# Performance work log

Hardware: AMD Instinct MI355X
Metric: run time of the kernel (lower is better)

Reference implementation:

```python
import jax, jax.numpy as jnp
import numpy as np

NUM_HEADS = 12


def setup_inputs() -> dict:
    key = jax.random.key(0)
    k0, k1, k2 = jax.random.split(key, 3)
    B, S, D = 2, 2048, 1536
    scale = 1.0 / np.sqrt(D)
    return {
        "hidden_states": jax.random.normal(k0, (B, S, D), dtype=jnp.float32),
        "W_fc": jax.random.normal(k1, (D, D), dtype=jnp.float32) * scale,
        "b_fc": jnp.zeros((D,), dtype=jnp.float32),
        "W_proj": jax.random.normal(k2, (D, D), dtype=jnp.float32) * scale,
        "b_proj": jnp.zeros((D,), dtype=jnp.float32),
    }


def reference(hidden_states, W_fc, b_fc, W_proj, b_proj):
    B, S, D = hidden_states.shape
    H = NUM_HEADS
    hd = D // H
    # value_states: [B, H, S, hd] (key_states == value_states in the original)
    v = (hidden_states @ W_fc.T + b_fc).reshape(B, S, H, hd).transpose(0, 2, 1, 3)
    # Uniform-weight causal sliding-window attention, window_h = 2^(h+1)-1.
    i = jnp.arange(S)[:, None]          # query pos
    j = jnp.arange(S)[None, :]          # key pos
    w = (2 ** jnp.arange(1, H + 1, dtype=jnp.int32) - 1)[:, None, None]  # [H,1,1]
    mask = (j <= i) & (j >= i - w + 1)                                    # [H,S,S]
    valid_len = jnp.minimum(i + 1, w).astype(v.dtype)                     # [H,S,1]
    attn = jnp.where(mask, 1.0 / valid_len, 0.0)                          # [H,S,S]
    # [H,S,S] x [B,H,S,hd] -> [B,S,H,hd] -> [B,S,D]
    out = jnp.einsum("hqk,bhkd->bqhd", attn, v).reshape(B, S, D)
    attn_weights = jnp.broadcast_to(attn[None], (B, H, S, S))
    return out @ W_proj.T + b_proj, attn_weights
```

## Files before the change

### kernel.cpp

```cpp
#include <hip/hip_runtime.h>
#include <hip/hip_bf16.h>

#define S_LEN   2048
#define DMODEL  1536
#define NBATCH  2
#define NHEADS  12
#define MROWS   (NBATCH * S_LEN)
#define NCHUNK  64
#define CHUNK   32

typedef unsigned short u16;
typedef __attribute__((ext_vector_type(8))) short bf16x8;
typedef __attribute__((ext_vector_type(4))) float f32x4;

__device__ __forceinline__ u16 f2bf(float x) {
  unsigned u = __float_as_uint(x);
  u += 0x7fffu + ((u >> 16) & 1u);
  return (u16)(u >> 16);
}
__device__ __forceinline__ float bf2f(u16 x) {
  return __uint_as_float(((unsigned)x) << 16);
}

#define N4_HID  1572864
#define N4_W    589824
__global__ void cvt_all(const float4* __restrict__ h, const float4* __restrict__ wf,
                        const float4* __restrict__ wp, ushort4* __restrict__ ho,
                        ushort4* __restrict__ wfo, ushort4* __restrict__ wpo) {
  int t = blockIdx.x * blockDim.x + threadIdx.x;
  const float4* src;
  ushort4* dst;
  int idx;
  if (t < N4_HID)            { src = h;  dst = ho;  idx = t; }
  else if (t < N4_HID + N4_W){ src = wf; dst = wfo; idx = t - N4_HID; }
  else                       { src = wp; dst = wpo; idx = t - N4_HID - N4_W; }
  float4 f = src[idx];
  ushort4 o;
  o.x = f2bf(f.x); o.y = f2bf(f.y); o.z = f2bf(f.z); o.w = f2bf(f.w);
  dst[idx] = o;
}

__device__ __forceinline__ void gld_lds16(u16* lds, const u16* g) {
  __builtin_amdgcn_global_load_lds(
      (const __attribute__((address_space(1))) unsigned int*)g,
      (__attribute__((address_space(3))) unsigned int*)lds, 16, 0, 0);
}

template <bool WITH_CSUM, typename CT>
__global__ __launch_bounds__(256)
void gemm_bt_bias(const u16* __restrict__ A, const u16* __restrict__ B,
                  const float* __restrict__ bias, CT* __restrict__ C,
                  float* __restrict__ cs, int Ndim, int Kdim) {
  __shared__ __align__(16) u16 As[128 * 32];
  __shared__ __align__(16) u16 Bs[128 * 32];
  __shared__ float colpart[4][128];

  const int tid  = threadIdx.x;
  const int wave = tid >> 6;
  const int lane = tid & 63;
  const int l15  = lane & 15;
  const int quad = lane >> 4;
  const int bm = blockIdx.y * 128;
  const int bn = blockIdx.x * 128;
  const int wm = (wave >> 1) * 64;
  const int wn = (wave & 1) * 64;

  f32x4 acc[4][4] = {};

  const int srow = wave * 32 + (lane >> 2);
  const int skk  = (lane & 3) * 8;
  const u16* gA = A + (size_t)(bm + srow) * Kdim + skk;
  const u16* gB = B + (size_t)(bn + srow) * Kdim + skk;
  u16* lA = &As[(wave * 32) * 32];
  u16* lB = &Bs[(wave * 32) * 32];
  const size_t rstep16 = (size_t)16 * Kdim;

  for (int k0 = 0; k0 < Kdim; k0 += 32) {
    gld_lds16(lA,           gA + k0);
    gld_lds16(lA + 16 * 32, gA + k0 + rstep16);
    gld_lds16(lB,           gB + k0);
    gld_lds16(lB + 16 * 32, gB + k0 + rstep16);
    __syncthreads();

    bf16x8 af[4], bfr[4];
#pragma unroll
    for (int i = 0; i < 4; ++i)
      af[i] = *(const bf16x8*)&As[(wm + i * 16 + l15) * 32 + quad * 8];
#pragma unroll
    for (int j = 0; j < 4; ++j)
      bfr[j] = *(const bf16x8*)&Bs[(wn + j * 16 + l15) * 32 + quad * 8];
#pragma unroll
    for (int i = 0; i < 4; ++i)
#pragma unroll
      for (int j = 0; j < 4; ++j)
        acc[i][j] = __builtin_amdgcn_mfma_f32_16x16x32_bf16(af[i], bfr[j], acc[i][j], 0, 0, 0);
    __syncthreads();
  }

  const int r0 = quad * 4;
#pragma unroll
  for (int j = 0; j < 4; ++j) {
    const int col = bn + wn + j * 16 + l15;
    const float bj = bias[col];
    float sA = 0.f, sB = 0.f;
#pragma unroll
    for (int i = 0; i < 4; ++i) {
      const int row = bm + wm + i * 16 + r0;
#pragma unroll
      for (int r = 0; r < 4; ++r) {
        float cv = acc[i][j][r] + bj;
        if constexpr (sizeof(CT) == 2)
          C[(size_t)(row + r) * Ndim + col] = (CT)f2bf(cv);
        else
          C[(size_t)(row + r) * Ndim + col] = (CT)cv;
        if (WITH_CSUM) { if (i < 2) sA += cv; else sB += cv; }
      }
    }
    if (WITH_CSUM) {
      sA += __shfl_xor(sA, 16); sA += __shfl_xor(sA, 32);
      sB += __shfl_xor(sB, 16); sB += __shfl_xor(sB, 32);
      if (quad == 0) {
        colpart[(wm >> 5) | 0][wn + j * 16 + l15] = sA;
        colpart[(wm >> 5) | 1][wn + j * 16 + l15] = sB;
      }
    }
  }
  if (WITH_CSUM) {
    __syncthreads();
    if (tid < 128) {
      const int b  = bm >> 11;
      const int c0 = (bm & 2047) >> 5;
#pragma unroll
      for (int g = 0; g < 4; ++g)
        cs[((size_t)b * NCHUNK + c0 + g) * DMODEL + bn + tid] = colpart[g][tid];
    }
  }
}

__global__ void chunk_prefix(const float* __restrict__ cs, float* __restrict__ E) {
  int t = blockIdx.x * blockDim.x + threadIdx.x;
  int d = t % DMODEL;
  int c = (t / DMODEL) % NCHUNK;
  int b = t / (DMODEL * NCHUNK);
  const float* p = cs + (size_t)b * NCHUNK * DMODEL + d;
  float s = 0.f;
  for (int cc = 0; cc < c; ++cc) s += p[(size_t)cc * DMODEL];
  E[t] = s;
}

__global__ void winavg_strip(const u16* __restrict__ v, const float* __restrict__ E,
                             u16* __restrict__ A2) {
  int t = blockIdx.x * blockDim.x + threadIdx.x;
  int d = t % DMODEL;
  int s = (t / DMODEL) & 255;
  int b = t / (DMODEL * 256);
  const int h = d >> 7;
  const int w = (2 << h) - 1;
  const u16* vb  = v + (size_t)b * S_LEN * DMODEL + d;
  const float* Eb = E + (size_t)b * NCHUNK * DMODEL + d;

  const int i0 = s * 8;
  float lead = Eb[(size_t)(i0 >> 5) * DMODEL];
  for (int r = i0 & ~31; r < i0; ++r)
    lead += bf2f(vb[(size_t)r * DMODEL]);

  float trail = 0.f;
  if (i0 + 7 >= w) {
    const int jf = max(i0, w) - w;
    if (jf > 0) {
      const int ct = (jf - 1) >> 5;
      trail = Eb[(size_t)ct * DMODEL];
      for (int r = ct * 32; r < jf; ++r)
        trail += bf2f(vb[(size_t)r * DMODEL]);
    }
  }

  u16* out = A2 + ((size_t)(b * S_LEN + i0)) * DMODEL + d;
#pragma unroll
  for (int rr = 0; rr < 8; ++rr) {
    const int i = i0 + rr;
    lead += bf2f(vb[(size_t)i * DMODEL]);
    float o;
    if (i < w) {
      o = lead / (float)(i + 1);
    } else {
      trail += bf2f(vb[(size_t)(i - w) * DMODEL]);
      o = (lead - trail) / (float)w;
    }
    out[(size_t)rr * DMODEL] = f2bf(o);
  }
}

__global__ void attn_weights_kernel(f32x4* __restrict__ out4) {
  int t = blockIdx.x * blockDim.x + threadIdx.x;
  int j0 = (t & 511) << 2;
  int i  = (t >> 9) & (S_LEN - 1);
  int bh = t >> 20;
  int h  = bh >= NHEADS ? bh - NHEADS : bh;
  int w  = (2 << h) - 1;
  int len = min(i + 1, w);
  float inv = 1.0f / (float)len;
  int lo = i - w + 1;
  f32x4 r;
  r.x = (j0     <= i && j0     >= lo) ? inv : 0.f;
  r.y = (j0 + 1 <= i && j0 + 1 >= lo) ? inv : 0.f;
  r.z = (j0 + 2 <= i && j0 + 2 >= lo) ? inv : 0.f;
  r.w = (j0 + 3 <= i && j0 + 3 >= lo) ? inv : 0.f;
  __builtin_nontemporal_store(r, &out4[t]);
}

extern "C" void kernel_launch(void* const* d_in, const int* in_sizes, int n_in,
                              void* d_out, int out_size, void* d_ws, size_t ws_size,
                              hipStream_t stream) {
  const float* hidden = (const float*)d_in[0];
  const float* W_fc   = (const float*)d_in[1];
  const float* b_fc   = (const float*)d_in[2];
  const float* W_proj = (const float*)d_in[3];
  const float* b_proj = (const float*)d_in[4];
  float* outp = (float*)d_out;

  char* ws = (char*)d_ws;
  u16*   A16   = (u16*)(ws);
  u16*   Wfc16 = (u16*)(ws + 12582912);
  u16*   Wpj16 = (u16*)(ws + 17301504);
  u16*   v16   = (u16*)(ws + 22020096);
  float* csums = (float*)(ws + 34603008);
  float* Epre  = (float*)(ws + 35389440);

  cvt_all<<<10752, 256, 0, stream>>>((const float4*)hidden, (const float4*)W_fc,
                                     (const float4*)W_proj, (ushort4*)A16,
                                     (ushort4*)Wfc16, (ushort4*)Wpj16);

  gemm_bt_bias<true, u16><<<dim3(DMODEL / 128, MROWS / 128), 256, 0, stream>>>(
      A16, Wfc16, b_fc, v16, csums, DMODEL, DMODEL);

  chunk_prefix<<<(NBATCH * NCHUNK * DMODEL) / 256, 256, 0, stream>>>(csums, Epre);

  winavg_strip<<<(NBATCH * (S_LEN / 8) * DMODEL) / 256, 256, 0, stream>>>(v16, Epre, A16);

  gemm_bt_bias<false, float><<<dim3(DMODEL / 128, MROWS / 128), 256, 0, stream>>>(
      A16, Wpj16, b_proj, outp, nullptr, DMODEL, DMODEL);

  attn_weights_kernel<<<(NBATCH * NHEADS * S_LEN * S_LEN / 4) / 256, 256, 0, stream>>>(
      (f32x4*)(outp + (size_t)MROWS * DMODEL));
}
```

Measured before the change: 574.6 us.

## Fuse attention-weights fill into both GEMM launches as extra blocks

Drops the standalone attention-weights kernel and appends 3072 extra blocks to each GEMM launch; these extra blocks run a grid-stride loop that writes half of the 400MB attention-weight tensor each. The goal is to overlap the bandwidth-bound weight writes with the compute-bound GEMMs and save one launch. GEMM tile indices move to a 1D grid. The risk is that store traffic competes with the GEMM loads, and scheduling may place the weight blocks after the GEMM blocks instead of alongside them.

New measurement: 541.1 us. 5.8% less time.

```diff
diff --git a/kernel.cpp b/kernel.cpp
--- a/kernel.cpp
+++ b/kernel.cpp
@@ -8,6 +8,11 @@
 #define MROWS   (NBATCH * S_LEN)
 #define NCHUNK  64
 #define CHUNK   32
+
+#define NGEMM_BLK  384
+#define AW_BLK     3072
+#define AW_TOTAL4  25165824u
+#define AW_HALF4   12582912u
 
 typedef unsigned short u16;
 typedef __attribute__((ext_vector_type(8))) short bf16x8;
@@ -48,9 +53,33 @@
 
 template <bool WITH_CSUM, typename CT>
 __global__ __launch_bounds__(256)
-void gemm_bt_bias(const u16* __restrict__ A, const u16* __restrict__ B,
-                  const float* __restrict__ bias, CT* __restrict__ C,
-                  float* __restrict__ cs, int Ndim, int Kdim) {
+void gemm_aw(const u16* __restrict__ A, const u16* __restrict__ B,
+             const float* __restrict__ bias, CT* __restrict__ C,
+             float* __restrict__ cs, f32x4* __restrict__ aw,
+             unsigned aw0, unsigned awcnt, int Ndim, int Kdim) {
+  if ((int)blockIdx.x >= NGEMM_BLK) {
+    const unsigned stride = (gridDim.x - NGEMM_BLK) * 256u;
+    const unsigned end = aw0 + awcnt;
+    unsigned t = aw0 + (blockIdx.x - NGEMM_BLK) * 256u + threadIdx.x;
+    for (; t < end; t += stride) {
+      int j0 = (int)(t & 511u) << 2;
+      int i  = (int)(t >> 9) & (S_LEN - 1);
+      int bh = (int)(t >> 20);
+      int h  = bh >= NHEADS ? bh - NHEADS : bh;
+      int w  = (2 << h) - 1;
+      int len = min(i + 1, w);
+      float inv = 1.0f / (float)len;
+      int lo = i - w + 1;
+      f32x4 r;
+      r.x = (j0     <= i && j0     >= lo) ? inv : 0.f;
+      r.y = (j0 + 1 <= i && j0 + 1 >= lo) ? inv : 0.f;
+      r.z = (j0 + 2 <= i && j0 + 2 >= lo) ? inv : 0.f;
+      r.w = (j0 + 3 <= i && j0 + 3 >= lo) ? inv : 0.f;
+      __builtin_nontemporal_store(r, &aw[t]);
+    }
+    return;
+  }
+
   __shared__ __align__(16) u16 As[128 * 32];
   __shared__ __align__(16) u16 Bs[128 * 32];
   __shared__ float colpart[4][128];
@@ -60,8 +89,8 @@
   const int lane = tid & 63;
   const int l15  = lane & 15;
   const int quad = lane >> 4;
-  const int bm = blockIdx.y * 128;
-  const int bn = blockIdx.x * 128;
+  const int bm = (blockIdx.x / (DMODEL / 128)) * 128;
+  const int bn = (blockIdx.x % (DMODEL / 128)) * 128;
   const int wm = (wave >> 1) * 64;
   const int wn = (wave & 1) * 64;
 
@@ -191,24 +220,6 @@
   }
 }
 
-__global__ void attn_weights_kernel(f32x4* __restrict__ out4) {
-  int t = blockIdx.x * blockDim.x + threadIdx.x;
-  int j0 = (t & 511) << 2;
-  int i  = (t >> 9) & (S_LEN - 1);
-  int bh = t >> 20;
-  int h  = bh >= NHEADS ? bh - NHEADS : bh;
-  int w  = (2 << h) - 1;
-  int len = min(i + 1, w);
-  float inv = 1.0f / (float)len;
-  int lo = i - w + 1;
-  f32x4 r;
-  r.x = (j0     <= i && j0     >= lo) ? inv : 0.f;
-  r.y = (j0 + 1 <= i && j0 + 1 >= lo) ? inv : 0.f;
-  r.z = (j0 + 2 <= i && j0 + 2 >= lo) ? inv : 0.f;
-  r.w = (j0 + 3 <= i && j0 + 3 >= lo) ? inv : 0.f;
-  __builtin_nontemporal_store(r, &out4[t]);
-}
-
 extern "C" void kernel_launch(void* const* d_in, const int* in_sizes, int n_in,
                               void* d_out, int out_size, void* d_ws, size_t ws_size,
                               hipStream_t stream) {
@@ -218,6 +229,7 @@
   const float* W_proj = (const float*)d_in[3];
   const float* b_proj = (const float*)d_in[4];
   float* outp = (float*)d_out;
+  f32x4* aw = (f32x4*)(outp + (size_t)MROWS * DMODEL);
 
   char* ws = (char*)d_ws;
   u16*   A16   = (u16*)(ws);
@@ -231,16 +243,13 @@
                                      (const float4*)W_proj, (ushort4*)A16,
                                      (ushort4*)Wfc16, (ushort4*)Wpj16);
 
-  gemm_bt_bias<true, u16><<<dim3(DMODEL / 128, MROWS / 128), 256, 0, stream>>>(
-      A16, Wfc16, b_fc, v16, csums, DMODEL, DMODEL);
+  gemm_aw<true, u16><<<NGEMM_BLK + AW_BLK, 256, 0, stream>>>(
+      A16, Wfc16, b_fc, v16, csums, aw, 0u, AW_HALF4, DMODEL, DMODEL);
 
   chunk_prefix<<<(NBATCH * NCHUNK * DMODEL) / 256, 256, 0, stream>>>(csums, Epre);
 
   winavg_strip<<<(NBATCH * (S_LEN / 8) * DMODEL) / 256, 256, 0, stream>>>(v16, Epre, A16);
 
-  gemm_bt_bias<false, float><<<dim3(DMODEL / 128, MROWS / 128), 256, 0, stream>>>(
-      A16, Wpj16, b_proj, outp, nullptr, DMODEL, DMODEL);
-
-  attn_weights_kernel<<<(NBATCH * NHEADS * S_LEN * S_LEN / 4) / 256, 256, 0, stream>>>(
-      (f32x4*)(outp + (size_t)MROWS * DMODEL));
-}
+  gemm_aw<false, float><<<NGEMM_BLK + AW_BLK, 256, 0, stream>>>(
+      A16, Wpj16, b_proj, outp, nullptr, aw, AW_HALF4, AW_HALF4, DMODEL, DMODEL);
+}
```
